# Kernel optimization log

Hardware: AMD Instinct MI355X
Metric: run time of the kernel (lower is better)

The kernel has to match this reference:

```python
import jax, jax.numpy as jnp
import numpy as np

B, S, E = 8, 2048, 1024

def setup_inputs() -> dict:
    key = jax.random.key(0)
    ks = jax.random.split(key, 9)
    def xavier(k, shape):
        fan_in, fan_out = shape[1], shape[0]
        lim = (6.0 / (fan_in + fan_out)) ** 0.5
        return jax.random.uniform(k, shape, jnp.float32, -lim, lim)
    return {
        "queries": jax.random.normal(ks[0], (B, S, E), jnp.float32),
        "keys":    jax.random.normal(ks[1], (B, S, E), jnp.float32),
        "values":  jax.random.normal(ks[2], (B, S, E), jnp.float32),
        "Wq": xavier(ks[3], (E, E)), "bq": jnp.zeros((E,), jnp.float32),
        "Wk": xavier(ks[4], (E, E)), "bk": jnp.zeros((E,), jnp.float32),
        "Wv": xavier(ks[5], (E, E)), "bv": jnp.zeros((E,), jnp.float32),
    }

def reference(queries, keys, values, Wq, bq, Wk, bk, Wv, bv):
    # torch Linear: x @ W.T + b
    q = jnp.einsum('bse,fe->bsf', queries, Wq) + bq
    k = jnp.einsum('bse,fe->bsf', keys, Wk) + bk
    v = jnp.einsum('bse,fe->bsf', values, Wv) + bv
    d = q.shape[-1]
    scores = jnp.einsum('bqe,bke->bqk', q, k) / jnp.sqrt(jnp.float32(d))
    attn = jax.nn.softmax(scores, axis=-1)
    # dropout is identity at inference
    out = jnp.einsum('bqk,bke->bqe', attn, v)
    return jnp.squeeze(out, axis=1) if out.shape[1] == 1 else out
```

## Files before the change

kernel.cpp:

```cpp
#include <hip/hip_runtime.h>
#include <stdint.h>

typedef float f32x4 __attribute__((ext_vector_type(4)));
typedef __bf16 bf16x8 __attribute__((ext_vector_type(8)));

__device__ __forceinline__ uint16_t f2bf(float f) {
    uint32_t x = __builtin_bit_cast(uint32_t, f);
    uint32_t lsb = (x >> 16) & 1u;
    return (uint16_t)((x + 0x7fffu + lsb) >> 16);
}
__device__ __forceinline__ float bf2f(uint32_t u) {
    return __builtin_bit_cast(float, u << 16);
}

__device__ __forceinline__ void gload16(const uint16_t* g, const uint8_t* l) {
    __builtin_amdgcn_global_load_lds(
        (const __attribute__((address_space(1))) uint32_t*)g,
        (__attribute__((address_space(3))) uint32_t*)l,
        16, 0, 0);
}

__global__ __launch_bounds__(256) void zero_f32(float* __restrict__ p, int n) {
    int i = blockIdx.x * 256 + threadIdx.x;
    if (i < n) p[i] = 0.f;
}

__global__ __launch_bounds__(256) void cvt3_f32_bf16(
    const float* __restrict__ s0, const float* __restrict__ s1, const float* __restrict__ s2,
    uint16_t* __restrict__ d0, uint16_t* __restrict__ d1, uint16_t* __restrict__ d2, int n8)
{
    const float* src = (blockIdx.y == 0) ? s0 : (blockIdx.y == 1) ? s1 : s2;
    uint16_t*   dst = (blockIdx.y == 0) ? d0 : (blockIdx.y == 1) ? d1 : d2;
    int idx = blockIdx.x * 256 + threadIdx.x;
    int stride = gridDim.x * 256;
    for (int i = idx; i < n8; i += stride) {
        const float4* s = (const float4*)src + 2 * (size_t)i;
        float4 a = s[0], b = s[1];
        uint4 o;
        o.x = (uint32_t)f2bf(a.x) | ((uint32_t)f2bf(a.y) << 16);
        o.y = (uint32_t)f2bf(a.z) | ((uint32_t)f2bf(a.w) << 16);
        o.z = (uint32_t)f2bf(b.x) | ((uint32_t)f2bf(b.y) << 16);
        o.w = (uint32_t)f2bf(b.z) | ((uint32_t)f2bf(b.w) << 16);
        ((uint4*)dst)[i] = o;
    }
}

template<typename TO, int BIAS_MODE, int EPI>
__global__ __launch_bounds__(512, 2) void gemm256(
    const uint16_t* __restrict__ A, const uint16_t* __restrict__ Bm,
    const float* __restrict__ bias, float* __restrict__ lsum, TO* __restrict__ D,
    int lda, int ldb, int ldd, int K, int ntn,
    long long sA, long long sB, long long sD, float scale)
{
    __shared__ uint4 ldsq[6144];
    uint8_t* ldsb = (uint8_t*)ldsq;

    int bid = blockIdx.x;
    const int nx = gridDim.x;
    bid = (bid & 7) * (nx >> 3) + (bid >> 3);
    const int tm = bid / ntn, tn = bid % ntn;
    const int bz = blockIdx.y;
    A  += (size_t)bz * sA;
    Bm += (size_t)bz * sB;
    D  += (size_t)bz * sD;
    float* lz = (EPI != 0) ? (lsum + (size_t)bz * 2048) : nullptr;

    const int m0 = tm * 256, n0 = tn * 256;
    const int t = threadIdx.x;
    const int wid = t >> 6, lane = t & 63;
    const int wm = wid >> 2, wn = wid & 3;
    const int r16 = lane & 15, g = lane >> 4;

    const int lco = r16 * 64 + ((g ^ ((r16 >> 1) & 3)) << 4);

    const int sslot = (lane & 3) ^ ((lane >> 3) & 3);
    const int c0 = 2 * wid;
    const int gr0 = c0 * 16 + (lane >> 2);
    const uint16_t* aS0 = A  + (size_t)(m0 + gr0) * lda + sslot * 8;
    const uint16_t* aS1 = A  + (size_t)(m0 + gr0 + 16) * lda + sslot * 8;
    const uint16_t* bS0 = Bm + (size_t)(n0 + gr0) * ldb + sslot * 8;
    const uint16_t* bS1 = Bm + (size_t)(n0 + gr0 + 16) * ldb + sslot * 8;
    const int dA0 = c0 * 1024, dA1 = dA0 + 1024;

#define STAGE_A(sl, kk) do { uint8_t* _b = ldsb + (sl) * 32768; \
    gload16(aS0 + (kk), _b + dA0); gload16(aS1 + (kk), _b + dA1); } while (0)
#define STAGE_B(sl, kk) do { uint8_t* _b = ldsb + (sl) * 32768 + 16384; \
    gload16(bS0 + (kk), _b + dA0); gload16(bS1 + (kk), _b + dA1); } while (0)

    f32x4 acc[8][4];
#pragma unroll
    for (int i = 0; i < 8; ++i)
#pragma unroll
        for (int j = 0; j < 4; ++j)
            acc[i][j] = (f32x4){0.f, 0.f, 0.f, 0.f};

    const int NT = K >> 5;
    STAGE_A(0, 0); STAGE_B(0, 0);
    STAGE_A(1, 32); STAGE_B(1, 32);

    int s_cur = 0;
    for (int tt = 0; tt < NT; ++tt) {
        int s2 = s_cur + 2; if (s2 >= 3) s2 -= 3;
        int t2 = tt + 2; if (t2 >= NT) t2 -= NT;
        const int kk2 = t2 << 5;

        asm volatile("s_waitcnt vmcnt(4)" ::: "memory");
        __builtin_amdgcn_s_barrier();
        asm volatile("" ::: "memory");

        const uint8_t* Ab = ldsb + s_cur * 32768 + wm * 8192;
        const uint8_t* Bb = ldsb + s_cur * 32768 + 16384 + wn * 4096;

        STAGE_A(s2, kk2);
        uint4 af[8], bfr[4];
#pragma unroll
        for (int m = 0; m < 8; ++m)
            af[m] = *(const uint4*)(Ab + m * 1024 + lco);
        bfr[0] = *(const uint4*)(Bb + lco);
        bfr[1] = *(const uint4*)(Bb + 1024 + lco);
        __builtin_amdgcn_s_setprio(1);
#pragma unroll
        for (int m = 0; m < 8; ++m) {
            acc[m][0] = __builtin_amdgcn_mfma_f32_16x16x32_bf16(
                __builtin_bit_cast(bf16x8, af[m]), __builtin_bit_cast(bf16x8, bfr[0]), acc[m][0], 0, 0, 0);
            acc[m][1] = __builtin_amdgcn_mfma_f32_16x16x32_bf16(
                __builtin_bit_cast(bf16x8, af[m]), __builtin_bit_cast(bf16x8, bfr[1]), acc[m][1], 0, 0, 0);
        }
        __builtin_amdgcn_s_setprio(0);

        STAGE_B(s2, kk2);
        bfr[2] = *(const uint4*)(Bb + 2048 + lco);
        bfr[3] = *(const uint4*)(Bb + 3072 + lco);
        __builtin_amdgcn_s_setprio(1);
#pragma unroll
        for (int m = 0; m < 8; ++m) {
            acc[m][2] = __builtin_amdgcn_mfma_f32_16x16x32_bf16(
                __builtin_bit_cast(bf16x8, af[m]), __builtin_bit_cast(bf16x8, bfr[2]), acc[m][2], 0, 0, 0);
            acc[m][3] = __builtin_amdgcn_mfma_f32_16x16x32_bf16(
                __builtin_bit_cast(bf16x8, af[m]), __builtin_bit_cast(bf16x8, bfr[3]), acc[m][3], 0, 0, 0);
        }
        __builtin_amdgcn_s_setprio(0);

        s_cur += 1; if (s_cur >= 3) s_cur = 0;
    }
#undef STAGE_A
#undef STAGE_B

#pragma unroll
    for (int mf = 0; mf < 8; ++mf) {
        const int grow0 = m0 + wm * 128 + mf * 16 + g * 4;
        float rs[4] = {0.f, 0.f, 0.f, 0.f};
        float invl[4];
        if constexpr (EPI == 2) {
#pragma unroll
            for (int r = 0; r < 4; ++r) invl[r] = 1.0f / lz[grow0 + r];
        }
#pragma unroll
        for (int nf = 0; nf < 4; ++nf) {
            const int gcol = n0 + wn * 64 + nf * 16 + r16;
            float bcol = (BIAS_MODE == 1) ? bias[gcol] : 0.f;
#pragma unroll
            for (int r = 0; r < 4; ++r) {
                float v = acc[mf][nf][r];
                float bb = (BIAS_MODE == 1) ? bcol : ((BIAS_MODE == 2) ? bias[grow0 + r] : 0.f);
                v = (v + bb) * scale;
                if constexpr (EPI == 0) {
                    if constexpr (sizeof(TO) == 2)
                        ((uint16_t*)D)[(size_t)(grow0 + r) * ldd + gcol] = f2bf(v);
                    else
                        ((float*)D)[(size_t)(grow0 + r) * ldd + gcol] = v;
                } else if constexpr (EPI == 1) {
                    float e = __expf(v);
                    uint16_t h = f2bf(e);
                    ((uint16_t*)D)[(size_t)(grow0 + r) * ldd + gcol] = h;
                    rs[r] += bf2f(h);
                } else {
                    ((float*)D)[(size_t)(grow0 + r) * ldd + gcol] = v * invl[r];
                }
            }
        }
        if constexpr (EPI == 1) {
#pragma unroll
            for (int r = 0; r < 4; ++r) {
                float s = rs[r];
                s += __shfl_xor(s, 1);
                s += __shfl_xor(s, 2);
                s += __shfl_xor(s, 4);
                s += __shfl_xor(s, 8);
                if ((lane & 15) == 0) atomicAdd(&lz[grow0 + r], s);
            }
        }
    }
}

extern "C" void kernel_launch(void* const* d_in, const int* in_sizes, int n_in,
                              void* d_out, int out_size, void* d_ws, size_t ws_size,
                              hipStream_t stream)
{
    const float* q_in = (const float*)d_in[0];
    const float* k_in = (const float*)d_in[1];
    const float* v_in = (const float*)d_in[2];
    const float* Wq   = (const float*)d_in[3];
    const float* bq   = (const float*)d_in[4];
    const float* Wk   = (const float*)d_in[5];
    const float* bk   = (const float*)d_in[6];
    const float* Wv   = (const float*)d_in[7];
    const float* bv   = (const float*)d_in[8];

    const size_t MS = (size_t)16384 * 1024;
    const size_t WS = (size_t)1024 * 1024;
    const size_t SS = (size_t)8 * 2048 * 2048;
    size_t needed = (3 * MS + SS) * sizeof(uint16_t) + 16384 * sizeof(float);
    if (ws_size < needed) return;

    uint16_t* Qb = (uint16_t*)d_ws;
    uint16_t* Kb = Qb + MS;
    uint16_t* VT = Kb + MS;
    uint16_t* Sc = VT + MS;
    float*    lrow = (float*)(Sc + SS);

    uint16_t* Xv  = Sc;
    uint16_t* Wqb = Sc + MS;
    uint16_t* Wkb = Wqb + WS;
    uint16_t* Wvb = Wkb + WS;
    uint16_t* Xq  = (uint16_t*)d_out;
    uint16_t* Xk  = Xq + MS;

    dim3 blk(256);
    dim3 blk5(512);

    zero_f32<<<dim3(64), blk, 0, stream>>>(lrow, 16384);

    cvt3_f32_bf16<<<dim3(1024, 3), blk, 0, stream>>>(
        q_in, k_in, v_in, Xq, Xk, Xv, (int)(MS / 8));
    cvt3_f32_bf16<<<dim3(128, 3), blk, 0, stream>>>(
        Wq, Wk, Wv, Wqb, Wkb, Wvb, (int)(WS / 8));

    gemm256<uint16_t, 1, 0><<<dim3(256, 1), blk5, 0, stream>>>(
        Xq, Wqb, bq, nullptr, Qb, 1024, 1024, 1024, 1024, 4, 0, 0, 0, 0.03125f);
    gemm256<uint16_t, 1, 0><<<dim3(256, 1), blk5, 0, stream>>>(
        Xk, Wkb, bk, nullptr, Kb, 1024, 1024, 1024, 1024, 4, 0, 0, 0, 1.0f);
    gemm256<uint16_t, 2, 0><<<dim3(32, 8), blk5, 0, stream>>>(
        Wvb, Xv, bv, nullptr, VT, 1024, 1024, 2048, 1024, 8,
        0, (long long)2048 * 1024, (long long)1024 * 2048, 1.0f);
    gemm256<uint16_t, 0, 1><<<dim3(64, 8), blk5, 0, stream>>>(
        Qb, Kb, nullptr, lrow, Sc, 1024, 1024, 2048, 1024, 8,
        (long long)2048 * 1024, (long long)2048 * 1024, (long long)2048 * 2048, 1.0f);
    gemm256<float, 0, 2><<<dim3(32, 8), blk5, 0, stream>>>(
        Sc, VT, nullptr, lrow, (float*)d_out, 2048, 2048, 1024, 2048, 4,
        (long long)2048 * 2048, (long long)1024 * 2048, (long long)2048 * 1024, 1.0f);
}
```

Baseline: 568.6 us.

## Deepen GEMM LDS pipeline to four stages with per-phase barrier interleaving

Grows the LDS ring buffer from three to four 32KB stages and lowers the launch-bounds occupancy hint from 2 to 1 blocks per CU. The main loop is restructured to issue global->LDS loads after fragment reads, with s_barrier and sched_barrier fences between each MFMA phase, in a ping-pong style schedule. The staging row mapping is also changed so each wave loads rows wid and wid+128. The aim is to overlap memory and MFMA across waves more tightly, at the cost of halved occupancy and more barriers per iteration.

```diff
diff --git a/kernel.cpp b/kernel.cpp
--- a/kernel.cpp
+++ b/kernel.cpp
@@ -45,14 +45,16 @@
     }
 }
 
+#define SCHED0() __builtin_amdgcn_sched_barrier(0)
+
 template<typename TO, int BIAS_MODE, int EPI>
-__global__ __launch_bounds__(512, 2) void gemm256(
+__global__ __launch_bounds__(512, 1) void gemm256(
     const uint16_t* __restrict__ A, const uint16_t* __restrict__ Bm,
     const float* __restrict__ bias, float* __restrict__ lsum, TO* __restrict__ D,
     int lda, int ldb, int ldd, int K, int ntn,
     long long sA, long long sB, long long sD, float scale)
 {
-    __shared__ uint4 ldsq[6144];
+    __shared__ uint4 ldsq[8192];
     uint8_t* ldsb = (uint8_t*)ldsq;
 
     int bid = blockIdx.x;
@@ -74,18 +76,12 @@
     const int lco = r16 * 64 + ((g ^ ((r16 >> 1) & 3)) << 4);
 
     const int sslot = (lane & 3) ^ ((lane >> 3) & 3);
-    const int c0 = 2 * wid;
-    const int gr0 = c0 * 16 + (lane >> 2);
+    const int gr0 = wid * 16 + (lane >> 2);
     const uint16_t* aS0 = A  + (size_t)(m0 + gr0) * lda + sslot * 8;
-    const uint16_t* aS1 = A  + (size_t)(m0 + gr0 + 16) * lda + sslot * 8;
+    const uint16_t* aS1 = A  + (size_t)(m0 + gr0 + 128) * lda + sslot * 8;
     const uint16_t* bS0 = Bm + (size_t)(n0 + gr0) * ldb + sslot * 8;
-    const uint16_t* bS1 = Bm + (size_t)(n0 + gr0 + 16) * ldb + sslot * 8;
-    const int dA0 = c0 * 1024, dA1 = dA0 + 1024;
-
-#define STAGE_A(sl, kk) do { uint8_t* _b = ldsb + (sl) * 32768; \
-    gload16(aS0 + (kk), _b + dA0); gload16(aS1 + (kk), _b + dA1); } while (0)
-#define STAGE_B(sl, kk) do { uint8_t* _b = ldsb + (sl) * 32768 + 16384; \
-    gload16(bS0 + (kk), _b + dA0); gload16(bS1 + (kk), _b + dA1); } while (0)
+    const uint16_t* bS1 = Bm + (size_t)(n0 + gr0 + 128) * ldb + sslot * 8;
+    const int dA0 = wid * 1024, dA1 = 8192 + wid * 1024;
 
     f32x4 acc[8][4];
 #pragma unroll
@@ -95,29 +91,42 @@
             acc[i][j] = (f32x4){0.f, 0.f, 0.f, 0.f};
 
     const int NT = K >> 5;
-    STAGE_A(0, 0); STAGE_B(0, 0);
-    STAGE_A(1, 32); STAGE_B(1, 32);
+
+    {
+        uint8_t* b0 = ldsb;
+        gload16(aS0, b0 + dA0); gload16(aS1, b0 + dA1);
+        gload16(bS0, b0 + 16384 + dA0); gload16(bS1, b0 + 16384 + dA1);
+        uint8_t* b1 = ldsb + 32768;
+        gload16(aS0 + 32, b1 + dA0); gload16(aS1 + 32, b1 + dA1);
+        gload16(bS0 + 32, b1 + 16384 + dA0); gload16(bS1 + 32, b1 + 16384 + dA1);
+    }
+    asm volatile("s_waitcnt vmcnt(4)" ::: "memory");
+    SCHED0();
+    __builtin_amdgcn_s_barrier();
+    SCHED0();
 
     int s_cur = 0;
     for (int tt = 0; tt < NT; ++tt) {
-        int s2 = s_cur + 2; if (s2 >= 3) s2 -= 3;
+        int s2 = s_cur + 2; if (s2 >= 4) s2 -= 4;
         int t2 = tt + 2; if (t2 >= NT) t2 -= NT;
         const int kk2 = t2 << 5;
 
-        asm volatile("s_waitcnt vmcnt(4)" ::: "memory");
-        __builtin_amdgcn_s_barrier();
-        asm volatile("" ::: "memory");
-
         const uint8_t* Ab = ldsb + s_cur * 32768 + wm * 8192;
         const uint8_t* Bb = ldsb + s_cur * 32768 + 16384 + wn * 4096;
-
-        STAGE_A(s2, kk2);
+        uint8_t* SA = ldsb + s2 * 32768;
+        uint8_t* SB = SA + 16384;
+
         uint4 af[8], bfr[4];
 #pragma unroll
         for (int m = 0; m < 8; ++m)
             af[m] = *(const uint4*)(Ab + m * 1024 + lco);
         bfr[0] = *(const uint4*)(Bb + lco);
         bfr[1] = *(const uint4*)(Bb + 1024 + lco);
+        gload16(aS0 + kk2, SA + dA0);
+        gload16(aS1 + kk2, SA + dA1);
+        SCHED0();
+        __builtin_amdgcn_s_barrier();
+        SCHED0();
         __builtin_amdgcn_s_setprio(1);
 #pragma unroll
         for (int m = 0; m < 8; ++m) {
@@ -127,10 +136,18 @@
                 __builtin_bit_cast(bf16x8, af[m]), __builtin_bit_cast(bf16x8, bfr[1]), acc[m][1], 0, 0, 0);
         }
         __builtin_amdgcn_s_setprio(0);
-
-        STAGE_B(s2, kk2);
+        SCHED0();
+        __builtin_amdgcn_s_barrier();
+        SCHED0();
+
         bfr[2] = *(const uint4*)(Bb + 2048 + lco);
         bfr[3] = *(const uint4*)(Bb + 3072 + lco);
+        gload16(bS0 + kk2, SB + dA0);
+        gload16(bS1 + kk2, SB + dA1);
+        asm volatile("s_waitcnt vmcnt(4)" ::: "memory");
+        SCHED0();
+        __builtin_amdgcn_s_barrier();
+        SCHED0();
         __builtin_amdgcn_s_setprio(1);
 #pragma unroll
         for (int m = 0; m < 8; ++m) {
@@ -140,11 +157,14 @@
                 __builtin_bit_cast(bf16x8, af[m]), __builtin_bit_cast(bf16x8, bfr[3]), acc[m][3], 0, 0, 0);
         }
         __builtin_amdgcn_s_setprio(0);
-
-        s_cur += 1; if (s_cur >= 3) s_cur = 0;
-    }
-#undef STAGE_A
-#undef STAGE_B
+        SCHED0();
+        __builtin_amdgcn_s_barrier();
+        SCHED0();
+
+        s_cur += 1; if (s_cur >= 4) s_cur = 0;
+    }
+    asm volatile("s_waitcnt vmcnt(0)" ::: "memory");
+    SCHED0();
 
 #pragma unroll
     for (int mf = 0; mf < 8; ++mf) {
```

Measured after the change: 523.4 us. 7.9% less time.
